# Kernel optimization log

Measured on AMD Instinct MI355X. Metric: run time of the kernel, lower is better.

The kernel has to match this reference:

```python
import jax, jax.numpy as jnp
import numpy as np

B, T, D, H = 64, 4096, 128, 256

def setup_inputs() -> dict:
    key = jax.random.key(0)
    ks = jax.random.split(key, 4)
    x = jax.random.normal(ks[0], (B, T, D), dtype=jnp.float32)
    Wx = jax.random.normal(ks[1], (D, H), dtype=jnp.float32) * (1.0 / np.sqrt(D))
    bx = jax.random.normal(ks[2], (H,), dtype=jnp.float32) * 0.02
    Wh = jax.random.normal(ks[3], (H, H), dtype=jnp.float32) * (1.0 / np.sqrt(H))
    bh = jnp.zeros((H,), dtype=jnp.float32)
    return {"x": x, "Wx": Wx, "bx": bx, "Wh": Wh, "bh": bh}

def reference(x, Wx, bx, Wh, bh):
    # Precompute input projections in one batched matmul: [B, T, H]
    xp = jnp.einsum('btd,dh->bth', x, Wx) + bx
    h0 = jnp.zeros((x.shape[0], Wh.shape[0]), dtype=x.dtype)

    def step(h, xp_t):
        # h: [B, H], xp_t: [B, H]
        h_new = jnp.tanh(xp_t + h @ Wh + bh)
        return h_new, h_new

    # scan over time: xp transposed to [T, B, H]
    _, h_seq = jax.lax.scan(step, h0, jnp.swapaxes(xp, 0, 1))
    return jnp.swapaxes(h_seq, 0, 1)  # [B, T, H]
```

## Files before the change

### kernel.cpp

```cpp
#include <hip/hip_runtime.h>

#define B_ 64
#define T_ 4096
#define D_ 128
#define H_ 256

__device__ __forceinline__ void barrier_lgkm() {
    asm volatile("s_waitcnt lgkmcnt(0)" ::: "memory");
    __builtin_amdgcn_s_barrier();
    asm volatile("" ::: "memory");
}

__global__ __launch_bounds__(1024) void xp_kernel(const float* __restrict__ x,
                                                  const float* __restrict__ Wx,
                                                  const float* __restrict__ bx,
                                                  float* __restrict__ out) {
    __shared__ float xs[64 * D_];
    const int tid = threadIdx.x;
    const int j = tid & 255;
    const int q = tid >> 8;
    const long row0 = (long)blockIdx.x * 64;

    const float4* xg = (const float4*)(x + row0 * D_);
    float4* xs4 = (float4*)xs;
    for (int i = tid; i < (64 * D_) / 4; i += 1024) xs4[i] = xg[i];
    __syncthreads();

    float acc[16];
#pragma unroll
    for (int r = 0; r < 16; ++r) acc[r] = 0.f;

    for (int k0 = 0; k0 < D_; k0 += 4) {
        const float w0 = Wx[(k0 + 0) * H_ + j];
        const float w1 = Wx[(k0 + 1) * H_ + j];
        const float w2 = Wx[(k0 + 2) * H_ + j];
        const float w3 = Wx[(k0 + 3) * H_ + j];
#pragma unroll
        for (int r = 0; r < 16; ++r) {
            const float4 xv = *(const float4*)(&xs[(q * 16 + r) * D_ + k0]);
            acc[r] += xv.x * w0 + xv.y * w1 + xv.z * w2 + xv.w * w3;
        }
    }

    const float bj = bx[j];
#pragma unroll
    for (int r = 0; r < 16; ++r) {
        out[(row0 + q * 16 + r) * H_ + j] = acc[r] + bj;
    }
}

__global__ __launch_bounds__(1024) void rnn_kernel(const float* __restrict__ Wh,
                                                   const float* __restrict__ bh,
                                                   float* __restrict__ out) {
    const int b = blockIdx.x;
    const int tid = threadIdx.x;
    const int j = tid & 255;
    const int q = tid >> 8;

    __shared__ float hs[H_];
    __shared__ float partial[3 * H_];

    float wreg[64];
#pragma unroll
    for (int ii = 0; ii < 64; ++ii) wreg[ii] = Wh[(q * 64 + ii) * H_ + j];
    const float bhj = bh[j];

    if (tid < H_) hs[tid] = 0.f;
    __syncthreads();

    float* obase = out + (long)b * T_ * H_;
    float xp0 = 0.f, xp1 = 0.f;
    if (q == 0) {
        xp0 = obase[j];
        xp1 = obase[H_ + j];
    }

#pragma unroll 2
    for (int t = 0; t < T_; ++t) {
        float xp2 = 0.f;
        if (q == 0 && t + 2 < T_) xp2 = obase[(long)(t + 2) * H_ + j];

        float a0 = 0.f, a1 = 0.f, a2 = 0.f, a3 = 0.f;
#pragma unroll
        for (int ii = 0; ii < 64; ii += 4) {
            const float4 hv = *(const float4*)(&hs[q * 64 + ii]);
            a0 += hv.x * wreg[ii + 0];
            a1 += hv.y * wreg[ii + 1];
            a2 += hv.z * wreg[ii + 2];
            a3 += hv.w * wreg[ii + 3];
        }
        const float p = (a0 + a1) + (a2 + a3);
        if (q != 0) partial[(q - 1) * H_ + j] = p;
        barrier_lgkm();

        if (q == 0) {
            float s = p + partial[j] + partial[H_ + j] + partial[2 * H_ + j]
                      + xp0 + bhj;
            s = fminf(15.f, fmaxf(-15.f, s));
            const float e = __expf(2.f * s);
            const float hn = __fdividef(e - 1.f, e + 1.f);
            hs[j] = hn;
            obase[(long)t * H_ + j] = hn;
            xp0 = xp1;
            xp1 = xp2;
        }
        barrier_lgkm();
    }
}

extern "C" void kernel_launch(void* const* d_in, const int* in_sizes, int n_in,
                              void* d_out, int out_size, void* d_ws, size_t ws_size,
                              hipStream_t stream) {
    const float* x  = (const float*)d_in[0];
    const float* Wx = (const float*)d_in[1];
    const float* bx = (const float*)d_in[2];
    const float* Wh = (const float*)d_in[3];
    const float* bh = (const float*)d_in[4];
    float* out = (float*)d_out;

    xp_kernel<<<(B_ * T_) / 64, 1024, 0, stream>>>(x, Wx, bx, out);
    rnn_kernel<<<B_, 1024, 0, stream>>>(Wh, bh, out);
}
```

Before: 3.710 ms.

## Repartition recurrent matvec into 16 K-slices with float4 output tiles per thread

The recurrent matvec is repartitioned so each of 16 wavefronts owns a 16-row K-slice of Wh, and each thread computes 4 output columns with float4 weights. Each h element read from LDS is now reused across 4 outputs, cutting LDS traffic per step. The cost is a larger 16-way partial-sum reduction done by 4 wavefronts, which adds LDS reads on the serial critical path between barriers.

Measured after the change: 3.687 ms. Within noise of the previous version (-0.6%).

```diff
diff --git a/kernel.cpp b/kernel.cpp
--- a/kernel.cpp
+++ b/kernel.cpp
@@ -54,53 +54,67 @@
                                                    float* __restrict__ out) {
     const int b = blockIdx.x;
     const int tid = threadIdx.x;
-    const int j = tid & 255;
-    const int q = tid >> 8;
+    const int lane = tid & 63;
+    const int s = tid >> 6;
+    const int j0 = lane << 2;
+    const int jr = ((s & 3) << 6) + lane;
 
     __shared__ float hs[H_];
-    __shared__ float partial[3 * H_];
+    __shared__ float partial[16][H_];
 
-    float wreg[64];
+    float4 wreg[16];
 #pragma unroll
-    for (int ii = 0; ii < 64; ++ii) wreg[ii] = Wh[(q * 64 + ii) * H_ + j];
-    const float bhj = bh[j];
+    for (int kk = 0; kk < 16; ++kk)
+        wreg[kk] = *(const float4*)(&Wh[(s * 16 + kk) * H_ + j0]);
+
+    const float bhj = bh[jr];
 
     if (tid < H_) hs[tid] = 0.f;
     __syncthreads();
 
     float* obase = out + (long)b * T_ * H_;
     float xp0 = 0.f, xp1 = 0.f;
-    if (q == 0) {
-        xp0 = obase[j];
-        xp1 = obase[H_ + j];
+    if (s < 4) {
+        xp0 = obase[jr];
+        xp1 = obase[H_ + jr];
     }
 
 #pragma unroll 2
     for (int t = 0; t < T_; ++t) {
         float xp2 = 0.f;
-        if (q == 0 && t + 2 < T_) xp2 = obase[(long)(t + 2) * H_ + j];
+        if (s < 4 && t + 2 < T_) xp2 = obase[(long)(t + 2) * H_ + jr];
 
-        float a0 = 0.f, a1 = 0.f, a2 = 0.f, a3 = 0.f;
+        float4 acc;
+        acc.x = 0.f; acc.y = 0.f; acc.z = 0.f; acc.w = 0.f;
+#define FMA4(HE, W) { const float he_ = (HE); const float4 w_ = (W); \
+        acc.x += he_ * w_.x; acc.y += he_ * w_.y;                     \
+        acc.z += he_ * w_.z; acc.w += he_ * w_.w; }
 #pragma unroll
-        for (int ii = 0; ii < 64; ii += 4) {
-            const float4 hv = *(const float4*)(&hs[q * 64 + ii]);
-            a0 += hv.x * wreg[ii + 0];
-            a1 += hv.y * wreg[ii + 1];
-            a2 += hv.z * wreg[ii + 2];
-            a3 += hv.w * wreg[ii + 3];
+        for (int c = 0; c < 4; ++c) {
+            const float4 hv = *(const float4*)(&hs[s * 16 + c * 4]);
+            FMA4(hv.x, wreg[c * 4 + 0])
+            FMA4(hv.y, wreg[c * 4 + 1])
+            FMA4(hv.z, wreg[c * 4 + 2])
+            FMA4(hv.w, wreg[c * 4 + 3])
         }
-        const float p = (a0 + a1) + (a2 + a3);
-        if (q != 0) partial[(q - 1) * H_ + j] = p;
+#undef FMA4
+        *(float4*)(&partial[s][j0]) = acc;
         barrier_lgkm();
 
-        if (q == 0) {
-            float s = p + partial[j] + partial[H_ + j] + partial[2 * H_ + j]
-                      + xp0 + bhj;
-            s = fminf(15.f, fmaxf(-15.f, s));
-            const float e = __expf(2.f * s);
+        if (s < 4) {
+            float v[16];
+#pragma unroll
+            for (int s2 = 0; s2 < 16; ++s2) v[s2] = partial[s2][jr];
+            const float t0 = (v[0] + v[1]) + (v[2] + v[3]);
+            const float t1 = (v[4] + v[5]) + (v[6] + v[7]);
+            const float t2 = (v[8] + v[9]) + (v[10] + v[11]);
+            const float t3 = (v[12] + v[13]) + (v[14] + v[15]);
+            float sum = ((t0 + t1) + (t2 + t3)) + (xp0 + bhj);
+            sum = fminf(15.f, fmaxf(-15.f, sum));
+            const float e = __expf(2.f * sum);
             const float hn = __fdividef(e - 1.f, e + 1.f);
-            hs[j] = hn;
-            obase[(long)t * H_ + j] = hn;
+            hs[jr] = hn;
+            obase[(long)t * H_ + jr] = hn;
             xp0 = xp1;
             xp1 = xp2;
         }
```

## Split RNN dot product across lane pairs with shuffle reduce and double-buffered h

Applied to the files above, without the earlier changes.

The recurrent kernel now runs 512 threads per batch row. Each output column is handled by two adjacent lanes that each cover half of the hidden dimension, and their partial sums are combined with a wavefront shuffle. This replaces the four-way split that wrote partials to shared memory. The hidden state is double-buffered in shared memory, so each timestep needs only one barrier instead of two, which shortens the serial per-step latency. The trade-offs are 128 weight registers per thread and half the lanes idle during the tanh/store phase.

Result: slower. 4.954 ms (+33.6%).

```diff
diff --git a/kernel.cpp b/kernel.cpp
--- a/kernel.cpp
+++ b/kernel.cpp
@@ -49,57 +49,64 @@
     }
 }
 
-__global__ __launch_bounds__(1024) void rnn_kernel(const float* __restrict__ Wh,
-                                                   const float* __restrict__ bh,
-                                                   float* __restrict__ out) {
+__global__ __launch_bounds__(512, 2) void rnn_kernel(const float* __restrict__ Wh,
+                                                     const float* __restrict__ bh,
+                                                     float* __restrict__ out) {
     const int b = blockIdx.x;
     const int tid = threadIdx.x;
-    const int j = tid & 255;
-    const int q = tid >> 8;
+    const int lane = tid & 63;
+    const int w = tid >> 6;
+    const int half = lane & 1;
+    const int j = (w << 5) + (lane >> 1);
+    const int kbase = half << 7;
 
-    __shared__ float hs[H_];
-    __shared__ float partial[3 * H_];
+    __shared__ float hs[2][H_];
 
-    float wreg[64];
+    float4 wreg[32];
 #pragma unroll
-    for (int ii = 0; ii < 64; ++ii) wreg[ii] = Wh[(q * 64 + ii) * H_ + j];
+    for (int c = 0; c < 32; ++c) {
+        wreg[c].x = Wh[(kbase + 4 * c + 0) * H_ + j];
+        wreg[c].y = Wh[(kbase + 4 * c + 1) * H_ + j];
+        wreg[c].z = Wh[(kbase + 4 * c + 2) * H_ + j];
+        wreg[c].w = Wh[(kbase + 4 * c + 3) * H_ + j];
+    }
     const float bhj = bh[j];
 
-    if (tid < H_) hs[tid] = 0.f;
+    ((float*)hs)[tid] = 0.f;
     __syncthreads();
 
     float* obase = out + (long)b * T_ * H_;
     float xp0 = 0.f, xp1 = 0.f;
-    if (q == 0) {
+    if (half == 0) {
         xp0 = obase[j];
         xp1 = obase[H_ + j];
     }
 
 #pragma unroll 2
     for (int t = 0; t < T_; ++t) {
+        const float* hb = hs[t & 1];
+
         float xp2 = 0.f;
-        if (q == 0 && t + 2 < T_) xp2 = obase[(long)(t + 2) * H_ + j];
+        if (half == 0 && t + 2 < T_) xp2 = obase[(long)(t + 2) * H_ + j];
 
         float a0 = 0.f, a1 = 0.f, a2 = 0.f, a3 = 0.f;
 #pragma unroll
-        for (int ii = 0; ii < 64; ii += 4) {
-            const float4 hv = *(const float4*)(&hs[q * 64 + ii]);
-            a0 += hv.x * wreg[ii + 0];
-            a1 += hv.y * wreg[ii + 1];
-            a2 += hv.z * wreg[ii + 2];
-            a3 += hv.w * wreg[ii + 3];
+        for (int c = 0; c < 32; ++c) {
+            const float4 hv = *(const float4*)(&hb[kbase + 4 * c]);
+            a0 += hv.x * wreg[c].x;
+            a1 += hv.y * wreg[c].y;
+            a2 += hv.z * wreg[c].z;
+            a3 += hv.w * wreg[c].w;
         }
-        const float p = (a0 + a1) + (a2 + a3);
-        if (q != 0) partial[(q - 1) * H_ + j] = p;
-        barrier_lgkm();
+        float p = (a0 + a1) + (a2 + a3);
+        p += __shfl_xor(p, 1, 64);
 
-        if (q == 0) {
-            float s = p + partial[j] + partial[H_ + j] + partial[2 * H_ + j]
-                      + xp0 + bhj;
-            s = fminf(15.f, fmaxf(-15.f, s));
-            const float e = __expf(2.f * s);
+        if (half == 0) {
+            float sum = p + xp0 + bhj;
+            sum = fminf(15.f, fmaxf(-15.f, sum));
+            const float e = __expf(2.f * sum);
             const float hn = __fdividef(e - 1.f, e + 1.f);
-            hs[j] = hn;
+            hs[(t + 1) & 1][j] = hn;
             obase[(long)t * H_ + j] = hn;
             xp0 = xp1;
             xp1 = xp2;
@@ -119,5 +126,5 @@
     float* out = (float*)d_out;
 
     xp_kernel<<<(B_ * T_) / 64, 1024, 0, stream>>>(x, Wx, bx, out);
-    rnn_kernel<<<B_, 1024, 0, stream>>>(Wh, bh, out);
+    rnn_kernel<<<B_, 512, 0, stream>>>(Wh, bh, out);
 }
```
